# Kernel tuning notes

Hardware: AMD Instinct MI355X
Metric: run time of the kernel (lower is better)

Reference implementation:

```python
import jax, jax.numpy as jnp
import numpy as np

H, W, DIM, NB = 64, 128, 768, 8
BS = DIM // NB
LAM = 0.01  # sparsity_threshold
EPS = 1e-5


def _layernorm(x, g, b):
    mu = jnp.mean(x, axis=-1, keepdims=True)
    var = jnp.mean(jnp.square(x - mu), axis=-1, keepdims=True)
    return (x - mu) * jax.lax.rsqrt(var + EPS) * g + b


def _softshrink(v):
    return jnp.sign(v) * jnp.maximum(jnp.abs(v) - LAM, 0.0)


def setup_inputs() -> dict:
    key = jax.random.key(0)
    ks = jax.random.split(key, 6)
    B = 4
    x = jax.random.normal(ks[0], (B, H * W, DIM), dtype=jnp.float32)
    w1 = 0.02 * jax.random.normal(ks[1], (NB, BS, BS), dtype=jnp.float32)
    b1 = 0.02 * jax.random.normal(ks[2], (NB, BS), dtype=jnp.float32)
    w2 = 0.02 * jax.random.normal(ks[3], (NB, BS, BS), dtype=jnp.float32)
    b2 = 0.02 * jax.random.normal(ks[4], (NB, BS), dtype=jnp.float32)
    km = jax.random.split(ks[5], 2)
    mlp_w1 = (1.0 / np.sqrt(DIM)) * jax.random.normal(km[0], (DIM, 4 * DIM), dtype=jnp.float32)
    mlp_w2 = (1.0 / np.sqrt(4 * DIM)) * jax.random.normal(km[1], (4 * DIM, DIM), dtype=jnp.float32)
    return {
        'x': x, 'w1': w1, 'b1': b1, 'w2': w2, 'b2': b2,
        'ln1_w': jnp.ones((DIM,), jnp.float32), 'ln1_b': jnp.zeros((DIM,), jnp.float32),
        'ln2_w': jnp.ones((DIM,), jnp.float32), 'ln2_b': jnp.zeros((DIM,), jnp.float32),
        'mlp_w1': mlp_w1, 'mlp_b1': jnp.zeros((4 * DIM,), jnp.float32),
        'mlp_w2': mlp_w2, 'mlp_b2': jnp.zeros((DIM,), jnp.float32),
    }


def reference(x, w1, b1, w2, b2, ln1_w, ln1_b, ln2_w, ln2_b, mlp_w1, mlp_b1, mlp_w2, mlp_b2):
    B = x.shape[0]
    xs = x.reshape(B, H, W, DIM)
    residual = xs
    xn = _layernorm(xs, ln1_w, ln1_b)
    xn = jnp.transpose(xn, (0, 3, 1, 2))  # [B, dim, h, w]
    xf = jnp.fft.rfft2(xn, norm='ortho')  # [B, dim, h, w//2+1] complex64
    Wf = xf.shape[-1]
    xf = xf.reshape(B, NB, BS, H, Wf)
    xr, xi = xf.real, xf.imag

    def bmm(t, Wm):  # block-diagonal matmul over feature dim j->m
        return jnp.einsum('bnjkl,njm->bnmkl', t, Wm)

    bb1 = b1[None, :, :, None, None]
    bb2 = b2[None, :, :, None, None]
    # NOTE: faithful to source -- both real and imag paths use the SAME weight matrix.
    o1r = jax.nn.relu(bmm(xr, w1) - bmm(xi, w1) + bb1)
    o1i = jax.nn.relu(bmm(xi, w1) + bmm(xr, w1) + bb1)
    o2r = bmm(o1r, w2) - bmm(o1i, w2) + bb2
    o2i = bmm(o1i, w2) + bmm(o1r, w2) + bb2
    o2 = _softshrink(o2r) + 1j * _softshrink(o2i)
    o2 = o2.reshape(B, DIM, H, Wf)
    xsp = jnp.fft.irfft2(o2, s=(H, W), norm='ortho')  # [B, dim, h, w]
    xsp = jnp.transpose(xsp, (0, 2, 3, 1)) + residual
    residual2 = xsp
    xn2 = _layernorm(xsp, ln2_w, ln2_b)
    hdd = jax.nn.gelu(xn2 @ mlp_w1 + mlp_b1, approximate=False)
    out = hdd @ mlp_w2 + mlp_b2 + residual2
    return out.reshape(B, H * W, DIM)
```

## Files before the change

### kernel.cpp

```cpp
#include <hip/hip_runtime.h>
#include <hip/hip_bf16.h>
#include <math.h>

#define B_    4
#define H_    64
#define W_    128
#define WF_   65
#define D_    768
#define NB_   8
#define BS_   96
#define HID_  3072
#define NTOK_ 32768
#define CHTOK_ 8192
#define LAM_  0.01f

typedef __hip_bfloat16 bf16;
typedef __attribute__((ext_vector_type(8))) short bf16x8;
typedef __attribute__((ext_vector_type(4))) float f32x4;
typedef unsigned int u32;

__device__ __forceinline__ float ldf(const float* p) { return *p; }
__device__ __forceinline__ float ldf(const bf16* p)  { return __bfloat162float(*p); }
__device__ __forceinline__ void stf(float* p, float v) { *p = v; }
__device__ __forceinline__ void stf(bf16* p, float v)  { *p = __float2bfloat16(v); }

#define GLOAD_LDS16(g, l) \
  __builtin_amdgcn_global_load_lds((const __attribute__((address_space(1))) u32*)(g), \
                                   (__attribute__((address_space(3))) u32*)(l), 16, 0, 0)

#define FRAG(arr, KP, row, kof) (*(const bf16x8*)((arr) + (size_t)(row) * (KP) + (kof)))

#define LUT_S1_OFF  0
#define LUT_S2M_OFF 22528
#define LUT_S2P_OFF 36864
#define LUT_S3_OFF  51200
#define LUT_TOTAL   77824

__global__ __launch_bounds__(256) void lut_init(bf16* __restrict__ lut) {
  const int idx = blockIdx.x * 256 + threadIdx.x;
  const float s1 = 0.011048543456039806f;
  float val = 0.f;
  if (idx < 22528) {
    int a = idx;
    if (a < 21760) {
      bool isC2 = a >= 10880; if (isC2) a -= 10880;
      int f = a / 136, w = a - f * 136;
      if (w < 128) {
        int p = (f * w) & 127;
        float ang = p * 0.04908738521234052f;
        val = isC2 ? -s1 * sinf(ang) : s1 * cosf(ang);
      }
    }
  } else if (idx < 51200) {
    int a = idx - 22528;
    float esign = -1.f;
    if (a >= 14336) { a -= 14336; esign = 1.f; }
    if (a < 13824) {
      int which = a / 4608; a -= which * 4608;
      int k = a / 72, h = a - k * 72;
      if (h < 64) {
        int p = (k * h) & 63;
        float ang = p * 0.09817477042468103f;
        float c = cosf(ang), s = esign * sinf(ang);
        val = (which == 0) ? c : ((which == 1) ? s : -s);
      }
    }
  } else {
    int a = idx - 51200;
    bool isCi = a >= 13312; if (isCi) a -= 13312;
    int w = a / 104, f = a - w * 104;
    if (f < WF_) {
      int p = (f * w) & 127;
      float ang = p * 0.04908738521234052f;
      float al = (f == 0 || f == 64) ? 1.0f : 2.0f;
      val = isCi ? -s1 * al * sinf(ang) : s1 * al * cosf(ang);
    }
  }
  lut[idx] = __float2bfloat16(val);
}

template <typename TIN>
__global__ __launch_bounds__(256) void ln_kernel(
    const TIN* __restrict__ x, const float* __restrict__ g,
    const float* __restrict__ bta, bf16* __restrict__ out) {
  __shared__ float sred[8];
  const size_t base = (size_t)blockIdx.x * D_;
  const int t = threadIdx.x;
  float v0 = ldf(x + base + t);
  float v1 = ldf(x + base + t + 256);
  float v2 = ldf(x + base + t + 512);
  float s = v0 + v1 + v2;
  #pragma unroll
  for (int o = 32; o; o >>= 1) s += __shfl_down(s, o, 64);
  int lane = t & 63, wid = t >> 6;
  if (lane == 0) sred[wid] = s;
  __syncthreads();
  if (t == 0) sred[0] = sred[0] + sred[1] + sred[2] + sred[3];
  __syncthreads();
  float mean = sred[0] * (1.0f / D_);
  float d0 = v0 - mean, d1 = v1 - mean, d2 = v2 - mean;
  float q = d0 * d0 + d1 * d1 + d2 * d2;
  #pragma unroll
  for (int o = 32; o; o >>= 1) q += __shfl_down(q, o, 64);
  if (lane == 0) sred[4 + wid] = q;
  __syncthreads();
  if (t == 0) sred[4] = sred[4] + sred[5] + sred[6] + sred[7];
  __syncthreads();
  float rstd = rsqrtf(sred[4] * (1.0f / D_) + 1e-5f);
  stf(out + base + t,       d0 * rstd * g[t]       + bta[t]);
  stf(out + base + t + 256, d1 * rstd * g[t + 256] + bta[t + 256]);
  stf(out + base + t + 512, d2 * rstd * g[t + 512] + bta[t + 512]);
}

__global__ __launch_bounds__(256) void s1_rfftw(
    const bf16* __restrict__ xn, const bf16* __restrict__ lut,
    bf16* __restrict__ fr, bf16* __restrict__ fi) {
  const int KP = 136;
  __shared__ __align__(16) bf16 sC[22528];
  __shared__ __align__(16) bf16 sXt[64 * 136];
  const int t = threadIdx.x;
  const int bh = blockIdx.x;
  const int c0 = blockIdx.y * 64;

  #pragma unroll
  for (int it = 0; it < 11; ++it)
    GLOAD_LDS16((const char*)lut + t * 16 + it * 4096, (char*)sC + t * 16 + it * 4096);

  {
    const int cv = (t & 7) * 8;
    #pragma unroll
    for (int rep = 0; rep < 4; ++rep) {
      int w = (t >> 3) + 32 * rep;
      bf16x8 v = *(const bf16x8*)(xn + ((size_t)bh * W_ + w) * D_ + c0 + cv);
      #pragma unroll
      for (int i = 0; i < 8; ++i) sXt[(cv + i) * KP + w] = ((const bf16*)&v)[i];
    }
  }
  __syncthreads();
  const bf16* sC1 = sC;
  const bf16* sC2 = sC + 10880;

  const int wave = t >> 6, lane = t & 63, l16 = lane & 15, quad = lane >> 4;
  const int ni = (wave == 0) ? 2 : 1;
  int itile[2] = {wave, 4};
  f32x4 accR[2][4], accI[2][4];
  #pragma unroll
  for (int ii = 0; ii < 2; ++ii)
    #pragma unroll
    for (int j = 0; j < 4; ++j) { accR[ii][j] = (f32x4){0,0,0,0}; accI[ii][j] = (f32x4){0,0,0,0}; }

  for (int s = 0; s < 4; ++s) {
    const int kof = s * 32 + quad * 8;
    bf16x8 bfrag[4];
    #pragma unroll
    for (int j = 0; j < 4; ++j) bfrag[j] = FRAG(sXt, KP, j * 16 + l16, kof);
    for (int ii = 0; ii < ni; ++ii) {
      const int arow = 16 * itile[ii] + l16;
      bf16x8 a1 = FRAG(sC1, KP, arow, kof);
      bf16x8 a2 = FRAG(sC2, KP, arow, kof);
      #pragma unroll
      for (int j = 0; j < 4; ++j) {
        accR[ii][j] = __builtin_amdgcn_mfma_f32_16x16x32_bf16(a1, bfrag[j], accR[ii][j], 0, 0, 0);
        accI[ii][j] = __builtin_amdgcn_mfma_f32_16x16x32_bf16(a2, bfrag[j], accI[ii][j], 0, 0, 0);
      }
    }
  }
  for (int ii = 0; ii < ni; ++ii) {
    #pragma unroll
    for (int r = 0; r < 4; ++r) {
      const int f = 16 * itile[ii] + quad * 4 + r;
      if (f >= WF_) continue;
      const size_t ob = ((size_t)bh * WF_ + f) * D_ + c0;
      #pragma unroll
      for (int j = 0; j < 4; ++j) {
        fr[ob + j * 16 + l16] = __float2bfloat16(accR[ii][j][r]);
        fi[ob + j * 16 + l16] = __float2bfloat16(accI[ii][j][r]);
      }
    }
  }
}

__global__ __launch_bounds__(256) void s2_ffth(
    const bf16* __restrict__ inr, const bf16* __restrict__ ini,
    bf16* __restrict__ outr, bf16* __restrict__ outi, const bf16* __restrict__ lut) {
  const int KP = 72;
  __shared__ __align__(16) bf16 sT[14336];
  __shared__ __align__(16) bf16 sFtr[64 * 72];
  __shared__ __align__(16) bf16 sFti[64 * 72];
  const int t = threadIdx.x;
  const int b = blockIdx.x / WF_;
  const int f = blockIdx.x % WF_;
  const int c0 = blockIdx.y * 64;

  #pragma unroll
  for (int it = 0; it < 7; ++it)
    GLOAD_LDS16((const char*)lut + t * 16 + it * 4096, (char*)sT + t * 16 + it * 4096);

  {
    const int cv = (t & 7) * 8;
    #pragma unroll
    for (int rep = 0; rep < 2; ++rep) {
      int h = (t >> 3) + 32 * rep;
      size_t g = ((size_t)(b * H_ + h) * WF_ + f) * D_ + c0 + cv;
      bf16x8 vr = *(const bf16x8*)(inr + g);
      bf16x8 vi = *(const bf16x8*)(ini + g);
      #pragma unroll
      for (int i = 0; i < 8; ++i) {
        sFtr[(cv + i) * KP + h] = ((const bf16*)&vr)[i];
        sFti[(cv + i) * KP + h] = ((const bf16*)&vi)[i];
      }
    }
  }
  __syncthreads();
  const bf16* sTr = sT;
  const bf16* sTi = sT + 4608;
  const bf16* sTn = sT + 9216;

  const int wave = t >> 6, lane = t & 63, l16 = lane & 15, quad = lane >> 4;
  f32x4 accR[4], accI[4];
  #pragma unroll
  for (int j = 0; j < 4; ++j) { accR[j] = (f32x4){0,0,0,0}; accI[j] = (f32x4){0,0,0,0}; }

  #pragma unroll
  for (int s = 0; s < 2; ++s) {
    const int kof = s * 32 + quad * 8;
    const int arow = 16 * wave + l16;
    bf16x8 ar = FRAG(sTr, KP, arow, kof);
    bf16x8 ai = FRAG(sTi, KP, arow, kof);
    bf16x8 an = FRAG(sTn, KP, arow, kof);
    #pragma unroll
    for (int j = 0; j < 4; ++j) {
      const int brow = j * 16 + l16;
      bf16x8 br = FRAG(sFtr, KP, brow, kof);
      bf16x8 bi = FRAG(sFti, KP, brow, kof);
      accR[j] = __builtin_amdgcn_mfma_f32_16x16x32_bf16(ar, br, accR[j], 0, 0, 0);
      accR[j] = __builtin_amdgcn_mfma_f32_16x16x32_bf16(an, bi, accR[j], 0, 0, 0);
      accI[j] = __builtin_amdgcn_mfma_f32_16x16x32_bf16(ai, br, accI[j], 0, 0, 0);
      accI[j] = __builtin_amdgcn_mfma_f32_16x16x32_bf16(ar, bi, accI[j], 0, 0, 0);
    }
  }
  #pragma unroll
  for (int r = 0; r < 4; ++r) {
    const int k = 16 * wave + quad * 4 + r;
    const size_t ob = ((size_t)(b * H_ + k) * WF_ + f) * D_ + c0;
    #pragma unroll
    for (int j = 0; j < 4; ++j) {
      outr[ob + j * 16 + l16] = __float2bfloat16(accR[j][r]);
      outi[ob + j * 16 + l16] = __float2bfloat16(accI[j][r]);
    }
  }
}

__global__ __launch_bounds__(256) void s3_irfftw(
    const bf16* __restrict__ fr, const bf16* __restrict__ fi,
    const bf16* __restrict__ lut, const float* __restrict__ x0, bf16* __restrict__ xsp) {
  const int KP = 104;
  __shared__ __align__(16) bf16 sC[26624];
  __shared__ __align__(16) bf16 sGtr[64 * 104];
  __shared__ __align__(16) bf16 sGti[64 * 104];
  const int t = threadIdx.x;
  const int bh = blockIdx.x;
  const int c0 = blockIdx.y * 64;

  #pragma unroll
  for (int it = 0; it < 13; ++it)
    GLOAD_LDS16((const char*)lut + t * 16 + it * 4096, (char*)sC + t * 16 + it * 4096);

  {
    const int cv = (t & 7) * 8;
    #pragma unroll
    for (int rep = 0; rep < 2; ++rep) {
      int f = (t >> 3) + 32 * rep;
      size_t g = ((size_t)bh * WF_ + f) * D_ + c0 + cv;
      bf16x8 vr = *(const bf16x8*)(fr + g);
      bf16x8 vi = *(const bf16x8*)(fi + g);
      #pragma unroll
      for (int i = 0; i < 8; ++i) {
        sGtr[(cv + i) * KP + f] = ((const bf16*)&vr)[i];
        sGti[(cv + i) * KP + f] = ((const bf16*)&vi)[i];
      }
    }
    if (t < 8) {
      size_t g = ((size_t)bh * WF_ + 64) * D_ + c0 + cv;
      bf16x8 vr = *(const bf16x8*)(fr + g);
      bf16x8 vi = *(const bf16x8*)(fi + g);
      #pragma unroll
      for (int i = 0; i < 8; ++i) {
        sGtr[(cv + i) * KP + 64] = ((const bf16*)&vr)[i];
        sGti[(cv + i) * KP + 64] = ((const bf16*)&vi)[i];
      }
    }
    const bf16 z = __float2bfloat16(0.f);
    for (int e = t; e < 64 * 31; e += 256) {
      int c = e / 31, f = 65 + (e - (e / 31) * 31);
      sGtr[c * KP + f] = z;
      sGti[c * KP + f] = z;
    }
  }
  __syncthreads();
  const bf16* sCr = sC;
  const bf16* sCi = sC + 13312;

  const int wave = t >> 6, lane = t & 63, l16 = lane & 15, quad = lane >> 4;
  f32x4 acc[2][4];
  #pragma unroll
  for (int ii = 0; ii < 2; ++ii)
    #pragma unroll
    for (int j = 0; j < 4; ++j) acc[ii][j] = (f32x4){0,0,0,0};

  #pragma unroll
  for (int s = 0; s < 3; ++s) {
    const int kof = s * 32 + quad * 8;
    bf16x8 br[4], bi[4];
    #pragma unroll
    for (int j = 0; j < 4; ++j) {
      br[j] = FRAG(sGtr, KP, j * 16 + l16, kof);
      bi[j] = FRAG(sGti, KP, j * 16 + l16, kof);
    }
    #pragma unroll
    for (int ii = 0; ii < 2; ++ii) {
      const int arow = 16 * (wave + 4 * ii) + l16;
      bf16x8 a1 = FRAG(sCr, KP, arow, kof);
      bf16x8 a2 = FRAG(sCi, KP, arow, kof);
      #pragma unroll
      for (int j = 0; j < 4; ++j) {
        acc[ii][j] = __builtin_amdgcn_mfma_f32_16x16x32_bf16(a1, br[j], acc[ii][j], 0, 0, 0);
        acc[ii][j] = __builtin_amdgcn_mfma_f32_16x16x32_bf16(a2, bi[j], acc[ii][j], 0, 0, 0);
      }
    }
  }
  #pragma unroll
  for (int ii = 0; ii < 2; ++ii) {
    #pragma unroll
    for (int r = 0; r < 4; ++r) {
      const int w = 16 * (wave + 4 * ii) + quad * 4 + r;
      const size_t ob = ((size_t)bh * W_ + w) * D_ + c0;
      #pragma unroll
      for (int j = 0; j < 4; ++j) {
        const size_t o = ob + j * 16 + l16;
        xsp[o] = __float2bfloat16(acc[ii][j][r] + x0[o]);
      }
    }
  }
}

__global__ __launch_bounds__(256) void blockmlp_mfma(
    bf16* __restrict__ gr, bf16* __restrict__ gi,
    const float* __restrict__ w1, const float* __restrict__ b1,
    const float* __restrict__ w2, const float* __restrict__ b2) {
  const int KP = 104;
  __shared__ __align__(16) bf16 sA[128 * 104];
  __shared__ __align__(16) bf16 sW[96 * 104];
  const int t = threadIdx.x;
  const int p0 = blockIdx.x * 64;
  const int nb = blockIdx.y;
  const int cbase = nb * BS_;

  #pragma unroll
  for (int it = 0; it < 3; ++it) {
    int task = t + 256 * it;
    int r = task / 12, jv = task - r * 12;
    size_t g = (size_t)(p0 + r) * D_ + cbase + jv * 8;
    bf16x8 vr = *(const bf16x8*)(gr + g);
    bf16x8 vi = *(const bf16x8*)(gi + g);
    bf16x8 u8, v8;
    #pragma unroll
    for (int i = 0; i < 8; ++i) {
      float xr = __bfloat162float(((const bf16*)&vr)[i]);
      float xi = __bfloat162float(((const bf16*)&vi)[i]);
      ((bf16*)&u8)[i] = __float2bfloat16(xr - xi);
      ((bf16*)&v8)[i] = __float2bfloat16(xr + xi);
    }
    *(bf16x8*)(sA + r * KP + jv * 8) = u8;
    *(bf16x8*)(sA + (64 + r) * KP + jv * 8) = v8;
  }
  {
    const float* wsrc = w1 + nb * BS_ * BS_;
    #pragma unroll
    for (int it = 0; it < 9; ++it) {
      int e4 = t + 256 * it;
      int j = e4 / 24, m4 = (e4 - j * 24) * 4;
      float4 ld = *(const float4*)(wsrc + j * 96 + m4);
      sW[(m4 + 0) * KP + j] = __float2bfloat16(ld.x);
      sW[(m4 + 1) * KP + j] = __float2bfloat16(ld.y);
      sW[(m4 + 2) * KP + j] = __float2bfloat16(ld.z);
      sW[(m4 + 3) * KP + j] = __float2bfloat16(ld.w);
    }
  }
  __syncthreads();

  const int wave = t >> 6, lane = t & 63, l16 = lane & 15, quad = lane >> 4;
  f32x4 accU[6], accV[6];
  #pragma unroll
  for (int n = 0; n < 6; ++n) { accU[n] = (f32x4){0,0,0,0}; accV[n] = (f32x4){0,0,0,0}; }

  #pragma unroll
  for (int s = 0; s < 3; ++s) {
    const int kof = s * 32 + quad * 8;
    bf16x8 au = FRAG(sA, KP, wave * 16 + l16, kof);
    bf16x8 av = FRAG(sA, KP, 64 + wave * 16 + l16, kof);
    bf16x8 bw[6];
    #pragma unroll
    for (int n = 0; n < 6; ++n) bw[n] = FRAG(sW, KP, n * 16 + l16, kof);
    #pragma unroll
    for (int n = 0; n < 6; ++n) {
      accU[n] = __builtin_amdgcn_mfma_f32_16x16x32_bf16(au, bw[n], accU[n], 0, 0, 0);
      accV[n] = __builtin_amdgcn_mfma_f32_16x16x32_bf16(av, bw[n], accV[n], 0, 0, 0);
    }
  }
  __syncthreads();

  {
    const float* wsrc = w2 + nb * BS_ * BS_;
    #pragma unroll
    for (int it = 0; it < 9; ++it) {
      int e4 = t + 256 * it;
      int j = e4 / 24, m4 = (e4 - j * 24) * 4;
      float4 ld = *(const float4*)(wsrc + j * 96 + m4);
      sW[(m4 + 0) * KP + j] = __float2bfloat16(ld.x);
      sW[(m4 + 1) * KP + j] = __float2bfloat16(ld.y);
      sW[(m4 + 2) * KP + j] = __float2bfloat16(ld.z);
      sW[(m4 + 3) * KP + j] = __float2bfloat16(ld.w);
    }
  }
  #pragma unroll
  for (int n = 0; n < 6; ++n) {
    const float bias = b1[cbase + n * 16 + l16];
    #pragma unroll
    for (int r = 0; r < 4; ++r) {
      float o1r = fmaxf(accU[n][r] + bias, 0.0f);
      float o1i = fmaxf(accV[n][r] + bias, 0.0f);
      const int row = wave * 16 + quad * 4 + r;
      sA[row * KP + n * 16 + l16]        = __float2bfloat16(o1r - o1i);
      sA[(64 + row) * KP + n * 16 + l16] = __float2bfloat16(o1r + o1i);
    }
  }
  __syncthreads();

  #pragma unroll
  for (int n = 0; n < 6; ++n) { accU[n] = (f32x4){0,0,0,0}; accV[n] = (f32x4){0,0,0,0}; }
  #pragma unroll
  for (int s = 0; s < 3; ++s) {
    const int kof = s * 32 + quad * 8;
    bf16x8 ap = FRAG(sA, KP, wave * 16 + l16, kof);
    bf16x8 aq = FRAG(sA, KP, 64 + wave * 16 + l16, kof);
    bf16x8 bw[6];
    #pragma unroll
    for (int n = 0; n < 6; ++n) bw[n] = FRAG(sW, KP, n * 16 + l16, kof);
    #pragma unroll
    for (int n = 0; n < 6; ++n) {
      accU[n] = __builtin_amdgcn_mfma_f32_16x16x32_bf16(ap, bw[n], accU[n], 0, 0, 0);
      accV[n] = __builtin_amdgcn_mfma_f32_16x16x32_bf16(aq, bw[n], accV[n], 0, 0, 0);
    }
  }

  #pragma unroll
  for (int n = 0; n < 6; ++n) {
    const float bias = b2[cbase + n * 16 + l16];
    #pragma unroll
    for (int r = 0; r < 4; ++r) {
      const int row = wave * 16 + quad * 4 + r;
      float o2r = accU[n][r] + bias;
      float o2i = accV[n][r] + bias;
      o2r = (o2r > LAM_) ? (o2r - LAM_) : ((o2r < -LAM_) ? (o2r + LAM_) : 0.0f);
      o2i = (o2i > LAM_) ? (o2i - LAM_) : ((o2i < -LAM_) ? (o2i + LAM_) : 0.0f);
      const size_t o = (size_t)(p0 + row) * D_ + cbase + n * 16 + l16;
      gr[o] = __float2bfloat16(o2r);
      gi[o] = __float2bfloat16(o2i);
    }
  }
}

__global__ __launch_bounds__(256) void wtrans_kernel(
    const float* __restrict__ Wm, bf16* __restrict__ Wt, int K, int N) {
  __shared__ float tile[32][33];
  const int n0 = blockIdx.x * 32;
  const int k0 = blockIdx.y * 32;
  const int tx = threadIdx.x & 31;
  const int ty = threadIdx.x >> 5;
  #pragma unroll
  for (int r = 0; r < 32; r += 8)
    tile[ty + r][tx] = Wm[(size_t)(k0 + ty + r) * N + n0 + tx];
  __syncthreads();
  #pragma unroll
  for (int r = 0; r < 32; r += 8)
    Wt[(size_t)(n0 + ty + r) * K + k0 + tx] = __float2bfloat16(tile[tx][ty + r]);
}

template <int MODE, typename TOUT>
__global__ __launch_bounds__(256) void mfma_gemm_kernel(
    const bf16* __restrict__ A, const bf16* __restrict__ Bt,
    const float* __restrict__ bias, const bf16* __restrict__ resid,
    TOUT* __restrict__ out, int M, int N, int K) {
  __shared__ __align__(16) bf16 As[128 * 32];
  __shared__ __align__(16) bf16 Bs[128 * 32];
  const int t = threadIdx.x;
  const int m0 = blockIdx.x * 128;
  const int n0 = blockIdx.y * 128;
  const int wave = t >> 6;
  const int lane = t & 63;
  const int wm = (wave & 1) * 64;
  const int wn = (wave >> 1) * 64;
  const int l16 = lane & 15;
  const int quad = lane >> 4;

  const int srow = t >> 2;
  const int skof = (t & 3) * 8;
  const bf16* Ag0 = A + (size_t)(m0 + srow) * K + skof;
  const bf16* Ag1 = A + (size_t)(m0 + 64 + srow) * K + skof;
  const bf16* Bg0 = Bt + (size_t)(n0 + srow) * K + skof;
  const bf16* Bg1 = Bt + (size_t)(n0 + 64 + srow) * K + skof;
  bf16* Al0 = As + t * 8;
  bf16* Al1 = As + 2048 + t * 8;
  bf16* Bl0 = Bs + t * 8;
  bf16* Bl1 = Bs + 2048 + t * 8;

  f32x4 acc[4][4];
  #pragma unroll
  for (int i = 0; i < 4; ++i)
    #pragma unroll
    for (int j = 0; j < 4; ++j) acc[i][j] = (f32x4){0.f, 0.f, 0.f, 0.f};

  for (int k0 = 0; k0 < K; k0 += 32) {
    __syncthreads();
    GLOAD_LDS16(Ag0 + k0, Al0);
    GLOAD_LDS16(Ag1 + k0, Al1);
    GLOAD_LDS16(Bg0 + k0, Bl0);
    GLOAD_LDS16(Bg1 + k0, Bl1);
    __syncthreads();
    bf16x8 af[4], bfr[4];
    #pragma unroll
    for (int i = 0; i < 4; ++i)
      af[i] = *(const bf16x8*)(As + (wm + i * 16 + l16) * 32 + quad * 8);
    #pragma unroll
    for (int j = 0; j < 4; ++j)
      bfr[j] = *(const bf16x8*)(Bs + (wn + j * 16 + l16) * 32 + quad * 8);
    #pragma unroll
    for (int i = 0; i < 4; ++i)
      #pragma unroll
      for (int j = 0; j < 4; ++j)
        acc[i][j] = __builtin_amdgcn_mfma_f32_16x16x32_bf16(af[i], bfr[j], acc[i][j], 0, 0, 0);
  }

  #pragma unroll
  for (int i = 0; i < 4; ++i) {
    #pragma unroll
    for (int j = 0; j < 4; ++j) {
      const int n = n0 + wn + j * 16 + l16;
      const float bz = bias[n];
      #pragma unroll
      for (int r = 0; r < 4; ++r) {
        const int m = m0 + wm + i * 16 + quad * 4 + r;
        float v = acc[i][j][r] + bz;
        if (MODE == 0) {
          v = 0.5f * v * (1.0f + erff(v * 0.70710678118654752f));
        } else {
          v += ldf(resid + (size_t)m * N + n);
        }
        stf(out + (size_t)m * N + n, v);
      }
    }
  }
}

extern "C" void kernel_launch(void* const* d_in, const int* in_sizes, int n_in,
                              void* d_out, int out_size, void* d_ws, size_t ws_size,
                              hipStream_t stream) {
  const float* x     = (const float*)d_in[0];
  const float* w1    = (const float*)d_in[1];
  const float* b1    = (const float*)d_in[2];
  const float* w2    = (const float*)d_in[3];
  const float* b2    = (const float*)d_in[4];
  const float* ln1w  = (const float*)d_in[5];
  const float* ln1b  = (const float*)d_in[6];
  const float* ln2w  = (const float*)d_in[7];
  const float* ln2b  = (const float*)d_in[8];
  const float* mlpw1 = (const float*)d_in[9];
  const float* mlpb1 = (const float*)d_in[10];
  const float* mlpw2 = (const float*)d_in[11];
  const float* mlpb2 = (const float*)d_in[12];
  float* out = (float*)d_out;

  const size_t SPA = (size_t)B_ * H_ * W_ * D_;
  const size_t FRE = (size_t)B_ * H_ * WF_ * D_;
  bf16* ws   = (bf16*)d_ws;
  bf16* bufA = ws;
  bf16* Fr   = bufA + SPA;
  bf16* Fi   = Fr + FRE;
  bf16* Gr   = Fi + FRE;
  bf16* Gi   = Gr + FRE;
  bf16* hid  = Fr;
  bf16* xn2c = Gr;
  bf16* w1t  = xn2c + (size_t)CHTOK_ * D_;
  bf16* w2t  = w1t + (size_t)D_ * HID_;

  bf16* lut = (bf16*)d_out;

  const int nspec = B_ * H_ * WF_;

  hipLaunchKernelGGL(lut_init, dim3(LUT_TOTAL / 256), dim3(256), 0, stream, lut);
  hipLaunchKernelGGL((ln_kernel<float>), dim3(NTOK_), dim3(256), 0, stream, x, ln1w, ln1b, bufA);
  hipLaunchKernelGGL(s1_rfftw, dim3(B_ * H_, D_ / 64), dim3(256), 0, stream,
                     bufA, lut + LUT_S1_OFF, Fr, Fi);
  hipLaunchKernelGGL(s2_ffth, dim3(B_ * WF_, D_ / 64), dim3(256), 0, stream,
                     Fr, Fi, Gr, Gi, lut + LUT_S2M_OFF);
  hipLaunchKernelGGL(blockmlp_mfma, dim3(nspec / 64, NB_), dim3(256), 0, stream,
                     Gr, Gi, w1, b1, w2, b2);
  hipLaunchKernelGGL(s2_ffth, dim3(B_ * WF_, D_ / 64), dim3(256), 0, stream,
                     Gr, Gi, Fr, Fi, lut + LUT_S2P_OFF);
  hipLaunchKernelGGL(s3_irfftw, dim3(B_ * H_, D_ / 64), dim3(256), 0, stream,
                     Fr, Fi, lut + LUT_S3_OFF, x, bufA);

  hipLaunchKernelGGL(wtrans_kernel, dim3(HID_ / 32, D_ / 32), dim3(256), 0, stream,
                     mlpw1, w1t, D_, HID_);
  hipLaunchKernelGGL(wtrans_kernel, dim3(D_ / 32, HID_ / 32), dim3(256), 0, stream,
                     mlpw2, w2t, HID_, D_);

  for (int c = 0; c < B_; ++c) {
    const bf16* rs = bufA + (size_t)c * CHTOK_ * D_;
    float* oc = out + (size_t)c * CHTOK_ * D_;
    hipLaunchKernelGGL((ln_kernel<bf16>), dim3(CHTOK_), dim3(256), 0, stream,
                       rs, ln2w, ln2b, xn2c);
    hipLaunchKernelGGL((mfma_gemm_kernel<0, bf16>), dim3(CHTOK_ / 128, HID_ / 128), dim3(256), 0,
                       stream, xn2c, w1t, mlpb1, (const bf16*)nullptr, hid, CHTOK_, HID_, D_);
    hipLaunchKernelGGL((mfma_gemm_kernel<1, float>), dim3(CHTOK_ / 128, D_ / 128), dim3(256), 0,
                       stream, hid, w2t, mlpb2, rs, oc, CHTOK_, D_, HID_);
  }
}
```

Before: 1.016 ms.

## Double-buffer GEMM LDS tiles, swizzle LDS layout, use tanh-approx GELU

The MFMA GEMM now double-buffers its A/B LDS tiles so the global-to-LDS loads for the next K step are issued before computing the current one, with a single barrier per iteration. It also applies an XOR swizzle to the LDS column offsets to reduce bank conflicts on fragment reads. The exact erf GELU is replaced by the tanh approximation computed via exp and a fast reciprocal, which changes numerics slightly and is not the exact GELU the reference uses. LDS usage doubles, which may reduce occupancy.

```diff
diff --git a/kernel.cpp b/kernel.cpp
--- a/kernel.cpp
+++ b/kernel.cpp
@@ -492,8 +492,8 @@
     const bf16* __restrict__ A, const bf16* __restrict__ Bt,
     const float* __restrict__ bias, const bf16* __restrict__ resid,
     TOUT* __restrict__ out, int M, int N, int K) {
-  __shared__ __align__(16) bf16 As[128 * 32];
-  __shared__ __align__(16) bf16 Bs[128 * 32];
+  __shared__ __align__(16) bf16 As[2][128 * 32];
+  __shared__ __align__(16) bf16 Bs[2][128 * 32];
   const int t = threadIdx.x;
   const int m0 = blockIdx.x * 128;
   const int n0 = blockIdx.y * 128;
@@ -505,15 +505,20 @@
   const int quad = lane >> 4;
 
   const int srow = t >> 2;
-  const int skof = (t & 3) * 8;
+  const int skof = ((t & 3) ^ ((srow >> 1) & 3)) * 8;
   const bf16* Ag0 = A + (size_t)(m0 + srow) * K + skof;
   const bf16* Ag1 = A + (size_t)(m0 + 64 + srow) * K + skof;
   const bf16* Bg0 = Bt + (size_t)(n0 + srow) * K + skof;
   const bf16* Bg1 = Bt + (size_t)(n0 + 64 + srow) * K + skof;
-  bf16* Al0 = As + t * 8;
-  bf16* Al1 = As + 2048 + t * 8;
-  bf16* Bl0 = Bs + t * 8;
-  bf16* Bl1 = Bs + 2048 + t * 8;
+
+  int aoff[4], boff[4];
+  #pragma unroll
+  for (int i = 0; i < 4; ++i) {
+    const int ra = wm + i * 16 + l16;
+    aoff[i] = ra * 32 + (quad ^ ((ra >> 1) & 3)) * 8;
+    const int rb = wn + i * 16 + l16;
+    boff[i] = rb * 32 + (quad ^ ((rb >> 1) & 3)) * 8;
+  }
 
   f32x4 acc[4][4];
   #pragma unroll
@@ -521,26 +526,42 @@
     #pragma unroll
     for (int j = 0; j < 4; ++j) acc[i][j] = (f32x4){0.f, 0.f, 0.f, 0.f};
 
-  for (int k0 = 0; k0 < K; k0 += 32) {
-    __syncthreads();
-    GLOAD_LDS16(Ag0 + k0, Al0);
-    GLOAD_LDS16(Ag1 + k0, Al1);
-    GLOAD_LDS16(Bg0 + k0, Bl0);
-    GLOAD_LDS16(Bg1 + k0, Bl1);
-    __syncthreads();
-    bf16x8 af[4], bfr[4];
-    #pragma unroll
-    for (int i = 0; i < 4; ++i)
-      af[i] = *(const bf16x8*)(As + (wm + i * 16 + l16) * 32 + quad * 8);
-    #pragma unroll
-    for (int j = 0; j < 4; ++j)
-      bfr[j] = *(const bf16x8*)(Bs + (wn + j * 16 + l16) * 32 + quad * 8);
-    #pragma unroll
-    for (int i = 0; i < 4; ++i)
-      #pragma unroll
-      for (int j = 0; j < 4; ++j)
-        acc[i][j] = __builtin_amdgcn_mfma_f32_16x16x32_bf16(af[i], bfr[j], acc[i][j], 0, 0, 0);
-  }
+#define STAGE_G(bb, ko) do { \
+    GLOAD_LDS16(Ag0 + (ko), &As[bb][t * 8]); \
+    GLOAD_LDS16(Ag1 + (ko), &As[bb][2048 + t * 8]); \
+    GLOAD_LDS16(Bg0 + (ko), &Bs[bb][t * 8]); \
+    GLOAD_LDS16(Bg1 + (ko), &Bs[bb][2048 + t * 8]); } while (0)
+
+#define COMPUTE_T(bb) do { \
+    bf16x8 af[4], bfr[4]; \
+    _Pragma("unroll") \
+    for (int i = 0; i < 4; ++i) af[i] = *(const bf16x8*)(As[bb] + aoff[i]); \
+    _Pragma("unroll") \
+    for (int j = 0; j < 4; ++j) bfr[j] = *(const bf16x8*)(Bs[bb] + boff[j]); \
+    _Pragma("unroll") \
+    for (int i = 0; i < 4; ++i) \
+      _Pragma("unroll") \
+      for (int j = 0; j < 4; ++j) \
+        acc[i][j] = __builtin_amdgcn_mfma_f32_16x16x32_bf16(af[i], bfr[j], acc[i][j], 0, 0, 0); \
+  } while (0)
+
+  const int NT = K >> 5;
+  STAGE_G(0, 0);
+  asm volatile("s_waitcnt vmcnt(0)" ::: "memory");
+  __builtin_amdgcn_s_barrier();
+  asm volatile("" ::: "memory");
+  int cur = 0;
+  for (int tt = 0; tt + 1 < NT; ++tt) {
+    STAGE_G(cur ^ 1, (tt + 1) << 5);
+    COMPUTE_T(cur);
+    asm volatile("s_waitcnt vmcnt(0)" ::: "memory");
+    __builtin_amdgcn_s_barrier();
+    asm volatile("" ::: "memory");
+    cur ^= 1;
+  }
+  COMPUTE_T(cur);
+#undef STAGE_G
+#undef COMPUTE_T
 
   #pragma unroll
   for (int i = 0; i < 4; ++i) {
@@ -553,7 +574,9 @@
         const int m = m0 + wm + i * 16 + quad * 4 + r;
         float v = acc[i][j][r] + bz;
         if (MODE == 0) {
-          v = 0.5f * v * (1.0f + erff(v * 0.70710678118654752f));
+          float q = v * fmaf(0.044715f, v * v, 1.0f);
+          float e = __expf(-1.5957691216f * q);
+          v = v * __builtin_amdgcn_rcpf(1.0f + e);
         } else {
           v += ldf(resid + (size_t)m * N + n);
         }
```

After: 945.3 us. 7.0% less time.
